# Performance work log

Measured on AMD Instinct MI355X. Metric: run time of the kernel, lower is better.

## Reference

```python
import jax, jax.numpy as jnp
import numpy as np

B, L, DM = 4, 2048, 1024
DI, DS, DR, K = 2 * DM, 16, 64, 4  # d_inner, d_state, dt_rank, d_conv


def setup_inputs() -> dict:
    key = jax.random.key(0)
    ks = jax.random.split(key, 10)
    # dt bias init as in Mamba: inv-softplus of dt ~ LogUniform(1e-3, 0.1)
    dt = jnp.exp(jax.random.uniform(ks[7], (DI,)) * (np.log(0.1) - np.log(1e-3)) + np.log(1e-3))
    dt = jnp.clip(dt, 1e-4, None)
    dt_proj_b = dt + jnp.log(-jnp.expm1(-dt))
    # A_log init: log(1..d_state) broadcast over d_inner
    A_log = jnp.log(jnp.broadcast_to(jnp.arange(1, DS + 1, dtype=jnp.float32), (DI, DS)))
    return {
        "hidden": jax.random.normal(ks[0], (B, L, DM), jnp.float32),
        "in_proj_w": jax.random.normal(ks[1], (2 * DI, DM), jnp.float32) * 0.02,
        "conv_w": jax.random.normal(ks[2], (DI, 1, K), jnp.float32) * 0.2,
        "conv_b": jax.random.normal(ks[3], (DI,), jnp.float32) * 0.02,
        "x_proj_w": jax.random.normal(ks[4], (DR + 2 * DS, DI), jnp.float32) * 0.02,
        "dt_proj_w": jax.random.normal(ks[5], (DI, DR), jnp.float32) * (DR ** -0.5),
        "dt_proj_b": dt_proj_b,
        "A_log": A_log,
        "D_param": jnp.ones((DI,), jnp.float32),
        "out_proj_w": jax.random.normal(ks[6], (DM, DI), jnp.float32) * 0.02,
    }


def reference(hidden, in_proj_w, conv_w, conv_b, x_proj_w, dt_proj_w, dt_proj_b, A_log, D_param, out_proj_w):
    b, l, dm = hidden.shape
    di = in_proj_w.shape[0] // 2
    ds = A_log.shape[1]
    dr = dt_proj_w.shape[1]
    k = conv_w.shape[-1]

    # in_proj (no bias): (b,l,2*di)
    xz = jnp.einsum('bld,ed->ble', hidden, in_proj_w)
    x, z = jnp.split(xz, 2, axis=-1)

    # causal depthwise conv1d over time + SiLU
    xt = x.transpose(0, 2, 1)  # (b, di, l)
    xc = jax.lax.conv_general_dilated(
        xt, conv_w, window_strides=(1,), padding=[(k - 1, 0)],
        feature_group_count=di, dimension_numbers=('NCH', 'OIH', 'NCH'))
    xc = jax.nn.silu(xc + conv_b[None, :, None])
    u = xc.transpose(0, 2, 1)  # (b, l, di)

    # input-dependent dt, B, C
    x_dbl = jnp.einsum('bld,ed->ble', u, x_proj_w)  # (b,l,dr+2*ds)
    dt, Bm, Cm = jnp.split(x_dbl, [dr, dr + ds], axis=-1)
    delta = jax.nn.softplus(jnp.einsum('blr,dr->bld', dt, dt_proj_w) + dt_proj_b)  # (b,l,di)

    A = -jnp.exp(A_log)  # (di, ds)

    def step(h, inp):
        dlt, Bt, Ct, ut = inp  # (b,di), (b,ds), (b,ds), (b,di)
        dA = jnp.exp(dlt[..., None] * A)               # (b,di,ds)
        h = dA * h + (dlt * ut)[..., None] * Bt[:, None, :]
        y = jnp.einsum('bdn,bn->bd', h, Ct)
        return h, y

    h0 = jnp.zeros((b, di, ds), hidden.dtype)
    xs = (delta.transpose(1, 0, 2), Bm.transpose(1, 0, 2),
          Cm.transpose(1, 0, 2), u.transpose(1, 0, 2))
    _, ys = jax.lax.scan(step, h0, xs)  # ys: (l,b,di)

    y = ys.transpose(1, 0, 2) + u * D_param  # skip connection
    y = y * jax.nn.silu(z)                   # gate
    return jnp.einsum('bld,od->blo', y, out_proj_w)
```

## Files before the change

### kernel.cpp

```cpp
#include <hip/hip_runtime.h>
#include <hip/hip_bf16.h>
#include <math.h>

#define BB 4
#define LL 2048
#define DM 1024
#define DI 2048
#define DS 16
#define DR 64
#define KC 4
#define TT (BB * LL)
#define NC 32
#define CL (LL / NC)
#define SK 8

typedef __hip_bfloat16 bf16;
typedef short bf16x8 __attribute__((ext_vector_type(8)));
typedef short short8 __attribute__((ext_vector_type(8)));
typedef float f32x4 __attribute__((ext_vector_type(4)));
typedef float float4v __attribute__((ext_vector_type(4)));

__device__ __forceinline__ float cvt(float v) { return v; }
__device__ __forceinline__ float cvt(bf16 v) { return __bfloat162float(v); }
__device__ __forceinline__ float bf2f(short s) {
  union { short s; bf16 h; } c; c.s = s; return __bfloat162float(c.h);
}
__device__ __forceinline__ void stv(float* p, float v) { *p = v; }
__device__ __forceinline__ void stv(bf16* p, float v) { *p = __float2bfloat16(v); }
__device__ __forceinline__ short f2bf(float f) {
  union { bf16 h; short s; } u_; u_.h = __float2bfloat16(f); return u_.s;
}

__device__ __forceinline__ void gld16(const bf16* g, bf16* l) {
  __builtin_amdgcn_global_load_lds(
      (const __attribute__((address_space(1))) void*)g,
      (__attribute__((address_space(3))) void*)l, 16, 0, 0);
}

__global__ __launch_bounds__(256) void cvt_bf16(
    const float* __restrict__ src, bf16* __restrict__ dst, int n8) {
  int i = blockIdx.x * 256 + threadIdx.x;
  if (i >= n8) return;
  const float4v* s = (const float4v*)(src + (size_t)i * 8);
  float4v v0 = s[0], v1 = s[1];
  short8 o;
#pragma unroll
  for (int j = 0; j < 4; ++j) { o[j] = f2bf(v0[j]); o[4 + j] = f2bf(v1[j]); }
  *(short8*)(dst + (size_t)i * 8) = o;
}

template <typename TC>
__global__ __launch_bounds__(256) void gemm_bf16(
    const bf16* __restrict__ A, int lda,
    const bf16* __restrict__ W, int ldw,
    TC* __restrict__ C, int ldc, int Kd) {
  __shared__ bf16 As[128 * 32];
  __shared__ bf16 Bs[128 * 32];
  int tid = threadIdx.x;
  int bm = blockIdx.y * 128, bn = blockIdx.x * 128;
  int wave = tid >> 6, lane = tid & 63;
  int wm = (wave >> 1) * 64, wn = (wave & 1) * 64;
  int lr = lane & 15, kg = lane >> 4;

  int srow = wave * 16 + (lane >> 2);
  int kc = (lane & 3) * 8;
  const bf16* gA0 = A + (size_t)(bm + srow) * lda + kc;
  const bf16* gA1 = gA0 + (size_t)64 * lda;
  const bf16* gW0 = W + (size_t)(bn + srow) * ldw + kc;
  const bf16* gW1 = gW0 + (size_t)64 * ldw;
  bf16* lA0 = &As[wave * 512];
  bf16* lA1 = &As[2048 + wave * 512];
  bf16* lB0 = &Bs[wave * 512];
  bf16* lB1 = &Bs[2048 + wave * 512];

  f32x4 acc[4][4] = {};

  for (int k0 = 0; k0 < Kd; k0 += 32) {
    __syncthreads();
    gld16(gA0 + k0, lA0);
    gld16(gA1 + k0, lA1);
    gld16(gW0 + k0, lB0);
    gld16(gW1 + k0, lB1);
    __syncthreads();

    bf16x8 af[4], bfr[4];
#pragma unroll
    for (int i = 0; i < 4; ++i)
      af[i] = *(const bf16x8*)&As[(wm + i * 16 + lr) * 32 + kg * 8];
#pragma unroll
    for (int j = 0; j < 4; ++j)
      bfr[j] = *(const bf16x8*)&Bs[(wn + j * 16 + lr) * 32 + kg * 8];
#pragma unroll
    for (int i = 0; i < 4; ++i)
#pragma unroll
      for (int j = 0; j < 4; ++j)
        acc[i][j] = __builtin_amdgcn_mfma_f32_16x16x32_bf16(af[i], bfr[j], acc[i][j], 0, 0, 0);
  }

#pragma unroll
  for (int i = 0; i < 4; ++i) {
    int row0 = bm + wm + i * 16 + kg * 4;
#pragma unroll
    for (int j = 0; j < 4; ++j) {
      int col = bn + wn + j * 16 + lr;
#pragma unroll
      for (int rr = 0; rr < 4; ++rr)
        stv(&C[(size_t)(row0 + rr) * ldc + col], acc[i][j][rr]);
    }
  }
}

__device__ __forceinline__ void loadcvt16(const float* p, short* d) {
#pragma unroll
  for (int i = 0; i < 4; ++i) {
    float4v v = ((const float4v*)p)[i];
#pragma unroll
    for (int j = 0; j < 4; ++j) d[i * 4 + j] = f2bf(v[j]);
  }
}
__device__ __forceinline__ void loadcvt16(const bf16* p, short* d) {
  ((short8*)d)[0] = ((const short8*)p)[0];
  ((short8*)d)[1] = ((const short8*)p)[1];
}

template <typename TA, typename TC, int EPI>
__global__ __launch_bounds__(256) void gemm_mfma(
    const TA* __restrict__ A, int lda,
    const float* __restrict__ W, int ldw,
    const float* __restrict__ bias,
    TC* __restrict__ C, int ldc, int Kd) {
  __shared__ short As[128 * 40];
  __shared__ short Bs[128 * 40];
  int tid = threadIdx.x;
  int bm = blockIdx.y * 128, bn = blockIdx.x * 128;

  int r = tid >> 1, hh = (tid & 1) * 16;
  const TA* ga = A + (size_t)(bm + r) * lda + hh;
  const float* gw = W + (size_t)(bn + r) * ldw + hh;

  int wave = tid >> 6, lane = tid & 63;
  int wm = (wave >> 1) * 64, wn = (wave & 1) * 64;
  int lr = lane & 15, kg = lane >> 4;

  f32x4 acc[4][4] = {};

  for (int k0 = 0; k0 < Kd; k0 += 32) {
    short abuf[16], wbuf[16];
    loadcvt16(ga + k0, abuf);
    loadcvt16(gw + k0, wbuf);
    __syncthreads();
    ((short8*)&As[r * 40 + hh])[0] = ((short8*)abuf)[0];
    ((short8*)&As[r * 40 + hh])[1] = ((short8*)abuf)[1];
    ((short8*)&Bs[r * 40 + hh])[0] = ((short8*)wbuf)[0];
    ((short8*)&Bs[r * 40 + hh])[1] = ((short8*)wbuf)[1];
    __syncthreads();

    bf16x8 af[4], bfr[4];
#pragma unroll
    for (int i = 0; i < 4; ++i)
      af[i] = *(const bf16x8*)&As[(wm + i * 16 + lr) * 40 + kg * 8];
#pragma unroll
    for (int j = 0; j < 4; ++j)
      bfr[j] = *(const bf16x8*)&Bs[(wn + j * 16 + lr) * 40 + kg * 8];
#pragma unroll
    for (int i = 0; i < 4; ++i)
#pragma unroll
      for (int j = 0; j < 4; ++j)
        acc[i][j] = __builtin_amdgcn_mfma_f32_16x16x32_bf16(af[i], bfr[j], acc[i][j], 0, 0, 0);
  }

#pragma unroll
  for (int i = 0; i < 4; ++i) {
    int row0 = bm + wm + i * 16 + kg * 4;
#pragma unroll
    for (int j = 0; j < 4; ++j) {
      int col = bn + wn + j * 16 + lr;
#pragma unroll
      for (int rr = 0; rr < 4; ++rr) {
        float v = acc[i][j][rr];
        if (EPI == 1) {
          v += bias[col];
          v = (v > 20.f) ? v : log1pf(expf(v));
        }
        stv(&C[(size_t)(row0 + rr) * ldc + col], v);
      }
    }
  }
}

__device__ __forceinline__ float* stslot(bf16* xz, int idx) {
  int t = idx >> 10, j = idx & 1023;
  return (float*)((char*)xz + (size_t)t * 8192) + j;
}
#define SUMD_BASE (8192 * NC * DS)

__global__ __launch_bounds__(256) void xproj_splitk(
    const bf16* __restrict__ u, const float* __restrict__ W,
    bf16* __restrict__ xz) {
  __shared__ short As[128 * 40];
  __shared__ short Bs[96 * 40];
  int tid = threadIdx.x;
  int bm = blockIdx.x * 128;
  int sk = blockIdx.y;
  int kb = sk * (DI / SK);

  int r = tid >> 1, hh = (tid & 1) * 16;
  const bf16* ga = u + (size_t)(bm + r) * DI + kb + hh;
  const float* gw = W + (size_t)r * DI + kb + hh;

  int wave = tid >> 6, lane = tid & 63;
  int wm = wave * 32;
  int lr = lane & 15, kg = lane >> 4;

  f32x4 acc[2][6] = {};

  for (int k0 = 0; k0 < DI / SK; k0 += 32) {
    short abuf[16], wbuf[16];
    loadcvt16(ga + k0, abuf);
    if (r < 96) loadcvt16(gw + k0, wbuf);
    __syncthreads();
    ((short8*)&As[r * 40 + hh])[0] = ((short8*)abuf)[0];
    ((short8*)&As[r * 40 + hh])[1] = ((short8*)abuf)[1];
    if (r < 96) {
      ((short8*)&Bs[r * 40 + hh])[0] = ((short8*)wbuf)[0];
      ((short8*)&Bs[r * 40 + hh])[1] = ((short8*)wbuf)[1];
    }
    __syncthreads();

    bf16x8 af[2], bfr[6];
#pragma unroll
    for (int i = 0; i < 2; ++i)
      af[i] = *(const bf16x8*)&As[(wm + i * 16 + lr) * 40 + kg * 8];
#pragma unroll
    for (int j = 0; j < 6; ++j)
      bfr[j] = *(const bf16x8*)&Bs[(j * 16 + lr) * 40 + kg * 8];
#pragma unroll
    for (int i = 0; i < 2; ++i)
#pragma unroll
      for (int j = 0; j < 6; ++j)
        acc[i][j] = __builtin_amdgcn_mfma_f32_16x16x32_bf16(af[i], bfr[j], acc[i][j], 0, 0, 0);
  }

#pragma unroll
  for (int i = 0; i < 2; ++i) {
#pragma unroll
    for (int j = 0; j < 6; ++j) {
      int col = j * 16 + lr;
#pragma unroll
      for (int rr = 0; rr < 4; ++rr) {
        int row = bm + wm + i * 16 + kg * 4 + rr;
        *stslot(xz, (sk * 8192 + row) * 96 + col) = acc[i][j][rr];
      }
    }
  }
}

__global__ __launch_bounds__(256) void xproj_reduce(
    bf16* __restrict__ xz, float* __restrict__ xdbl) {
  int gid = blockIdx.x * 256 + threadIdx.x;
  float s = 0.f;
#pragma unroll
  for (int sk = 0; sk < SK; ++sk)
    s += *stslot(xz, sk * (8192 * 96) + gid);
  xdbl[gid] = s;
}

__global__ __launch_bounds__(256) void conv_silu(
    const bf16* __restrict__ xz, const float* __restrict__ cw,
    const float* __restrict__ cb, bf16* __restrict__ u) {
  int t = blockIdx.x;
  int d0 = threadIdx.x * 8;
  int l = t & (LL - 1);

  float acc[8];
  float4v c0 = *(const float4v*)&cb[d0];
  float4v c1 = *(const float4v*)&cb[d0 + 4];
#pragma unroll
  for (int j = 0; j < 4; ++j) { acc[j] = c0[j]; acc[4 + j] = c1[j]; }

  float wv[32];
  const float4v* wp = (const float4v*)&cw[d0 * 4];
#pragma unroll
  for (int q = 0; q < 8; ++q) {
    float4v v = wp[q];
#pragma unroll
    for (int j = 0; j < 4; ++j) wv[q * 4 + j] = v[j];
  }

#pragma unroll
  for (int k = 0; k < KC; ++k) {
    int lt = l - (KC - 1) + k;
    if (lt >= 0) {
      short8 xv = *(const short8*)&xz[(size_t)(t - (KC - 1) + k) * (2 * DI) + d0];
#pragma unroll
      for (int q = 0; q < 8; ++q)
        acc[q] = fmaf(bf2f(xv[q]), wv[q * 4 + k], acc[q]);
    }
  }

  short8 ov;
#pragma unroll
  for (int q = 0; q < 8; ++q) {
    float s = acc[q] / (1.f + __expf(-acc[q]));
    ov[q] = f2bf(s);
  }
  *(short8*)&u[(size_t)t * DI + d0] = ov;
}

__global__ __launch_bounds__(256) void scan_local(
    const bf16* __restrict__ delta, const bf16* __restrict__ u,
    const float* __restrict__ xdbl, bf16* __restrict__ xz,
    const float* __restrict__ A_log) {
  int g = blockIdx.x * 256 + threadIdx.x;
  int d = g & (DI - 1);
  int b = (g >> 11) & (BB - 1);
  int c = g >> 13;
  int chain = (b << 11) | d;

  float Aj[DS];
  const float4v* Ap = (const float4v*)&A_log[d * DS];
#pragma unroll
  for (int i = 0; i < 4; ++i) {
    float4v v = Ap[i];
#pragma unroll
    for (int j = 0; j < 4; ++j) Aj[i * 4 + j] = -__expf(v[j]);
  }

  float h[DS];
#pragma unroll
  for (int s = 0; s < DS; ++s) h[s] = 0.f;
  float sd = 0.f;
  int t0 = b * LL + c * CL;

  for (int i = 0; i < CL; ++i) {
    int t = t0 + i;
    float dlt = cvt(delta[(size_t)t * DI + d]);
    float ut = cvt(u[(size_t)t * DI + d]);
    const float4v* Bp = (const float4v*)&xdbl[(size_t)t * (DR + 2 * DS) + DR];
    float Bv[DS];
#pragma unroll
    for (int q = 0; q < 4; ++q) {
      float4v v = Bp[q];
#pragma unroll
      for (int j = 0; j < 4; ++j) Bv[q * 4 + j] = v[j];
    }
    float du = dlt * ut;
    sd += dlt;
#pragma unroll
    for (int s = 0; s < DS; ++s)
      h[s] = fmaf(__expf(dlt * Aj[s]), h[s], du * Bv[s]);
  }

  float4v* hv = (float4v*)stslot(xz, (chain * NC + c) * DS);
#pragma unroll
  for (int q = 0; q < 4; ++q) {
    float4v v;
#pragma unroll
    for (int j = 0; j < 4; ++j) v[j] = h[q * 4 + j];
    hv[q] = v;
  }
  *stslot(xz, SUMD_BASE + chain * NC + c) = sd;
}

__global__ __launch_bounds__(256) void scan_fix(
    bf16* __restrict__ xz, const float* __restrict__ A_log) {
  int lane = threadIdx.x & 15;
  int chain = blockIdx.x * 16 + (threadIdx.x >> 4);
  int d = chain & (DI - 1);
  float Aj = -__expf(A_log[d * DS + lane]);
  float carry = 0.f;
  for (int c = 0; c < NC; ++c) {
    float* hp = stslot(xz, (chain * NC + c) * DS + lane);
    float sd = *stslot(xz, SUMD_BASE + chain * NC + c);
    float he = *hp;
    *hp = carry;
    carry = fmaf(__expf(Aj * sd), carry, he);
  }
}

__global__ __launch_bounds__(256) void scan_final(
    const bf16* __restrict__ delta, bf16* __restrict__ u,
    const float* __restrict__ xdbl, bf16* __restrict__ xz,
    const float* __restrict__ A_log, const float* __restrict__ Dp) {
  int g = blockIdx.x * 256 + threadIdx.x;
  int d = g & (DI - 1);
  int b = (g >> 11) & (BB - 1);
  int c = g >> 13;
  int chain = (b << 11) | d;

  float Aj[DS];
  const float4v* Ap = (const float4v*)&A_log[d * DS];
#pragma unroll
  for (int i = 0; i < 4; ++i) {
    float4v v = Ap[i];
#pragma unroll
    for (int j = 0; j < 4; ++j) Aj[i * 4 + j] = -__expf(v[j]);
  }
  float Dd = Dp[d];

  float h[DS];
  const float4v* hv = (const float4v*)stslot(xz, (chain * NC + c) * DS);
#pragma unroll
  for (int q = 0; q < 4; ++q) {
    float4v v = hv[q];
#pragma unroll
    for (int j = 0; j < 4; ++j) h[q * 4 + j] = v[j];
  }

  int t0 = b * LL + c * CL;
  for (int i = 0; i < CL; ++i) {
    int t = t0 + i;
    float dlt = cvt(delta[(size_t)t * DI + d]);
    float ut = cvt(u[(size_t)t * DI + d]);
    const float4v* Bp = (const float4v*)&xdbl[(size_t)t * (DR + 2 * DS) + DR];
    float BC[2 * DS];
#pragma unroll
    for (int q = 0; q < 8; ++q) {
      float4v v = Bp[q];
#pragma unroll
      for (int j = 0; j < 4; ++j) BC[q * 4 + j] = v[j];
    }
    float du = dlt * ut;
    float yp = 0.f;
#pragma unroll
    for (int s = 0; s < DS; ++s) {
      h[s] = fmaf(__expf(dlt * Aj[s]), h[s], du * BC[s]);
      yp = fmaf(h[s], BC[DS + s], yp);
    }
    float zt = cvt(xz[(size_t)t * (2 * DI) + DI + d]);
    float gte = zt / (1.f + __expf(-zt));
    stv(&u[(size_t)t * DI + d], (yp + ut * Dd) * gte);
  }
}

extern "C" void kernel_launch(void* const* d_in, const int* in_sizes, int n_in,
                              void* d_out, int out_size, void* d_ws, size_t ws_size,
                              hipStream_t stream) {
  const float* hidden    = (const float*)d_in[0];
  const float* in_proj_w = (const float*)d_in[1];
  const float* conv_w    = (const float*)d_in[2];
  const float* conv_b    = (const float*)d_in[3];
  const float* x_proj_w  = (const float*)d_in[4];
  const float* dt_proj_w = (const float*)d_in[5];
  const float* dt_proj_b = (const float*)d_in[6];
  const float* A_log     = (const float*)d_in[7];
  const float* D_param   = (const float*)d_in[8];
  const float* out_proj_w= (const float*)d_in[9];
  float* out = (float*)d_out;

  size_t need = (size_t)TT * 4096 * sizeof(bf16) + (size_t)TT * DI * sizeof(bf16)
              + (size_t)TT * (DR + 2 * DS) * sizeof(float) + (size_t)TT * DI * sizeof(bf16);
  if (ws_size < need) return;

  bf16* xz     = (bf16*)d_ws;
  bf16* u      = xz + (size_t)TT * 2 * DI;
  float* xdbl  = (float*)(u + (size_t)TT * DI);
  bf16* delta  = (bf16*)(xdbl + (size_t)TT * (DR + 2 * DS));

  bf16* hbf  = u;
  bf16* wbf  = u + (size_t)TT * DM;
  bf16* opbf = delta;

  dim3 blk(256);

  cvt_bf16<<<dim3(TT * DM / 8 / 256), blk, 0, stream>>>(hidden, hbf, TT * DM / 8);
  cvt_bf16<<<dim3(2 * DI * DM / 8 / 256), blk, 0, stream>>>(in_proj_w, wbf, 2 * DI * DM / 8);

  gemm_bf16<bf16><<<dim3(4096 / 128, TT / 128), blk, 0, stream>>>(
      hbf, DM, wbf, DM, xz, 2 * DI, DM);

  conv_silu<<<dim3(TT), blk, 0, stream>>>(xz, conv_w, conv_b, u);

  xproj_splitk<<<dim3(TT / 128, SK), blk, 0, stream>>>(u, x_proj_w, xz);
  xproj_reduce<<<dim3(TT * 96 / 256), blk, 0, stream>>>(xz, xdbl);

  gemm_mfma<float, bf16, 1><<<dim3(DI / 128, TT / 128), blk, 0, stream>>>(
      xdbl, DR + 2 * DS, dt_proj_w, DR, dt_proj_b, delta, DI, DR);

  scan_local<<<dim3(8192 * NC / 256), blk, 0, stream>>>(delta, u, xdbl, xz, A_log);
  scan_fix<<<dim3(8192 / 16), blk, 0, stream>>>(xz, A_log);
  scan_final<<<dim3(8192 * NC / 256), blk, 0, stream>>>(delta, u, xdbl, xz, A_log, D_param);

  cvt_bf16<<<dim3(DM * DI / 8 / 256), blk, 0, stream>>>(out_proj_w, opbf, DM * DI / 8);

  gemm_bf16<float><<<dim3(DM / 128, TT / 128), blk, 0, stream>>>(
      u, DI, opbf, DI, out, DM, DI);
}
```

Measured before the change: 535.2 us.

## Double-buffer bf16 GEMM LDS, pre-convert x_proj weights, unroll scan loops

The bf16 GEMM now uses two LDS buffers, so the next K-tile is loaded while MFMAs run on the current one, and one barrier per iteration is removed. x_proj weights are converted to bf16 once in a separate kernel, so the split-K xproj kernel no longer converts fp32 weights on every load. Both scan loops get unroll 2. LDS use in the GEMM doubles, which may lower occupancy, and the added conversion kernel adds a launch.

```diff
diff --git a/kernel.cpp b/kernel.cpp
--- a/kernel.cpp
+++ b/kernel.cpp
@@ -54,8 +54,8 @@
     const bf16* __restrict__ A, int lda,
     const bf16* __restrict__ W, int ldw,
     TC* __restrict__ C, int ldc, int Kd) {
-  __shared__ bf16 As[128 * 32];
-  __shared__ bf16 Bs[128 * 32];
+  __shared__ bf16 As[2][128 * 32];
+  __shared__ bf16 Bs[2][128 * 32];
   int tid = threadIdx.x;
   int bm = blockIdx.y * 128, bn = blockIdx.x * 128;
   int wave = tid >> 6, lane = tid & 63;
@@ -68,34 +68,40 @@
   const bf16* gA1 = gA0 + (size_t)64 * lda;
   const bf16* gW0 = W + (size_t)(bn + srow) * ldw + kc;
   const bf16* gW1 = gW0 + (size_t)64 * ldw;
-  bf16* lA0 = &As[wave * 512];
-  bf16* lA1 = &As[2048 + wave * 512];
-  bf16* lB0 = &Bs[wave * 512];
-  bf16* lB1 = &Bs[2048 + wave * 512];
 
   f32x4 acc[4][4] = {};
 
-  for (int k0 = 0; k0 < Kd; k0 += 32) {
+#define STAGE_BF(p, k0)                              \
+  do {                                               \
+    gld16(gA0 + (k0), &As[p][wave * 512]);           \
+    gld16(gA1 + (k0), &As[p][2048 + wave * 512]);    \
+    gld16(gW0 + (k0), &Bs[p][wave * 512]);           \
+    gld16(gW1 + (k0), &Bs[p][2048 + wave * 512]);    \
+  } while (0)
+
+#define COMPUTE_BF(p)                                                         \
+  do {                                                                        \
+    bf16x8 af[4], bfr[4];                                                     \
+    _Pragma("unroll") for (int i = 0; i < 4; ++i)                             \
+        af[i] = *(const bf16x8*)&As[p][(wm + i * 16 + lr) * 32 + kg * 8];     \
+    _Pragma("unroll") for (int j = 0; j < 4; ++j)                             \
+        bfr[j] = *(const bf16x8*)&Bs[p][(wn + j * 16 + lr) * 32 + kg * 8];    \
+    _Pragma("unroll") for (int i = 0; i < 4; ++i)                             \
+        _Pragma("unroll") for (int j = 0; j < 4; ++j)                         \
+            acc[i][j] = __builtin_amdgcn_mfma_f32_16x16x32_bf16(              \
+                af[i], bfr[j], acc[i][j], 0, 0, 0);                           \
+  } while (0)
+
+  STAGE_BF(0, 0);
+  __syncthreads();
+  int p = 0;
+  for (int k0 = 0; k0 < Kd - 32; k0 += 32) {
+    STAGE_BF(p ^ 1, k0 + 32);
+    COMPUTE_BF(p);
     __syncthreads();
-    gld16(gA0 + k0, lA0);
-    gld16(gA1 + k0, lA1);
-    gld16(gW0 + k0, lB0);
-    gld16(gW1 + k0, lB1);
-    __syncthreads();
-
-    bf16x8 af[4], bfr[4];
-#pragma unroll
-    for (int i = 0; i < 4; ++i)
-      af[i] = *(const bf16x8*)&As[(wm + i * 16 + lr) * 32 + kg * 8];
-#pragma unroll
-    for (int j = 0; j < 4; ++j)
-      bfr[j] = *(const bf16x8*)&Bs[(wn + j * 16 + lr) * 32 + kg * 8];
-#pragma unroll
-    for (int i = 0; i < 4; ++i)
-#pragma unroll
-      for (int j = 0; j < 4; ++j)
-        acc[i][j] = __builtin_amdgcn_mfma_f32_16x16x32_bf16(af[i], bfr[j], acc[i][j], 0, 0, 0);
-  }
+    p ^= 1;
+  }
+  COMPUTE_BF(p);
 
 #pragma unroll
   for (int i = 0; i < 4; ++i) {
@@ -108,6 +114,8 @@
         stv(&C[(size_t)(row0 + rr) * ldc + col], acc[i][j][rr]);
     }
   }
+#undef STAGE_BF
+#undef COMPUTE_BF
 }
 
 __device__ __forceinline__ void loadcvt16(const float* p, short* d) {
@@ -195,7 +203,7 @@
 #define SUMD_BASE (8192 * NC * DS)
 
 __global__ __launch_bounds__(256) void xproj_splitk(
-    const bf16* __restrict__ u, const float* __restrict__ W,
+    const bf16* __restrict__ u, const bf16* __restrict__ W,
     bf16* __restrict__ xz) {
   __shared__ short As[128 * 40];
   __shared__ short Bs[96 * 40];
@@ -206,7 +214,7 @@
 
   int r = tid >> 1, hh = (tid & 1) * 16;
   const bf16* ga = u + (size_t)(bm + r) * DI + kb + hh;
-  const float* gw = W + (size_t)r * DI + kb + hh;
+  const bf16* gw = W + (size_t)r * DI + kb + hh;
 
   int wave = tid >> 6, lane = tid & 63;
   int wm = wave * 32;
@@ -332,6 +340,7 @@
   float sd = 0.f;
   int t0 = b * LL + c * CL;
 
+#pragma unroll 2
   for (int i = 0; i < CL; ++i) {
     int t = t0 + i;
     float dlt = cvt(delta[(size_t)t * DI + d]);
@@ -408,6 +417,7 @@
   }
 
   int t0 = b * LL + c * CL;
+#pragma unroll 2
   for (int i = 0; i < CL; ++i) {
     int t = t0 + i;
     float dlt = cvt(delta[(size_t)t * DI + d]);
@@ -457,21 +467,23 @@
   float* xdbl  = (float*)(u + (size_t)TT * DI);
   bf16* delta  = (bf16*)(xdbl + (size_t)TT * (DR + 2 * DS));
 
-  bf16* hbf  = u;
-  bf16* wbf  = u + (size_t)TT * DM;
-  bf16* opbf = delta;
+  bf16* hbf   = u;
+  bf16* wbf   = u + (size_t)TT * DM;
+  bf16* wx_bf = delta;
+  bf16* opbf  = delta;
 
   dim3 blk(256);
 
   cvt_bf16<<<dim3(TT * DM / 8 / 256), blk, 0, stream>>>(hidden, hbf, TT * DM / 8);
   cvt_bf16<<<dim3(2 * DI * DM / 8 / 256), blk, 0, stream>>>(in_proj_w, wbf, 2 * DI * DM / 8);
+  cvt_bf16<<<dim3(96 * DI / 8 / 256), blk, 0, stream>>>(x_proj_w, wx_bf, 96 * DI / 8);
 
   gemm_bf16<bf16><<<dim3(4096 / 128, TT / 128), blk, 0, stream>>>(
       hbf, DM, wbf, DM, xz, 2 * DI, DM);
 
   conv_silu<<<dim3(TT), blk, 0, stream>>>(xz, conv_w, conv_b, u);
 
-  xproj_splitk<<<dim3(TT / 128, SK), blk, 0, stream>>>(u, x_proj_w, xz);
+  xproj_splitk<<<dim3(TT / 128, SK), blk, 0, stream>>>(u, wx_bf, xz);
   xproj_reduce<<<dim3(TT * 96 / 256), blk, 0, stream>>>(xz, xdbl);
 
   gemm_mfma<float, bf16, 1><<<dim3(DI / 128, TT / 128), blk, 0, stream>>>(
```

Measured after the change: 557.8 us. 1.04x slower.
